# Kernel tuning notes

Hardware: AMD Instinct MI355X
Metric: run time of the kernel (lower is better)

The kernel has to match this reference:

```python
import jax, jax.numpy as jnp
import numpy as np

B, S, H, I, E, TOP_K = 2, 2048, 1024, 2048, 8, 2


def setup_inputs() -> dict:
    key = jax.random.key(0)
    k1, k2, k3, k4, k5 = jax.random.split(key, 5)
    scale_h = 1.0 / np.sqrt(H)
    scale_i = 1.0 / np.sqrt(I)
    return {
        "hidden_states": jax.random.normal(k1, (B, S, H), dtype=jnp.float32),
        "router_w": jax.random.normal(k2, (H, E), dtype=jnp.float32) * scale_h,
        "gate_w": jax.random.normal(k3, (E, H, I), dtype=jnp.float32) * scale_h,
        "up_w": jax.random.normal(k4, (E, H, I), dtype=jnp.float32) * scale_h,
        "out_w": jax.random.normal(k5, (E, I, H), dtype=jnp.float32) * scale_i,
    }


def reference(hidden_states, router_w, gate_w, up_w, out_w):
    b, s, h = hidden_states.shape
    x = hidden_states.reshape(-1, h)  # [T, H], T = B*S

    # Router: logits -> softmax -> top-k -> renormalize -> dense routing matrix
    router_logits = x @ router_w  # [T, E]
    router_probs = jax.nn.softmax(router_logits, axis=-1)
    top_p, top_i = jax.lax.top_k(router_probs, TOP_K)  # [T, K]
    top_p = top_p / jnp.sum(top_p, axis=-1, keepdims=True)
    one_hot = jax.nn.one_hot(top_i, E, dtype=top_p.dtype)  # [T, K, E]
    routing_full = jnp.sum(one_hot * top_p[..., None], axis=1)  # [T, E]
    routing_full = routing_full.T  # [E, T]

    # Dense all-expert FFN (SwiGLU), as in the original batched einsum form
    gate = jnp.einsum("th,ehm->etm", x, gate_w)  # [E, T, I]
    gate = jax.nn.silu(gate)
    intermediate = jnp.einsum("th,ehm->etm", x, up_w)  # [E, T, I]
    hidden = intermediate * gate
    expert_out = jnp.einsum("eti,eih->eth", hidden, out_w)  # [E, T, H]

    # Weighted combine over experts
    out = jnp.sum(expert_out * routing_full[:, :, None], axis=0)  # [T, H]
    out = out.reshape(b, s, h)
    return out, router_logits
```

## Files before the change

### kernel.cpp

```cpp
#include <hip/hip_runtime.h>
#include <hip/hip_bf16.h>
#include <stdint.h>

#define TT 4096
#define HH 1024
#define II 2048
#define EE 8
#define RB 16
#define NRB (TT / RB)
#define CSTRIDE 32

typedef short bf16x8 __attribute__((ext_vector_type(8)));
typedef float f32x4 __attribute__((ext_vector_type(4)));

__device__ __forceinline__ unsigned short f2bf(float f) {
  unsigned u = __float_as_uint(f);
  u += 0x7FFF + ((u >> 16) & 1);
  return (unsigned short)(u >> 16);
}

__device__ __forceinline__ void gl_lds16(const void* g, void* l) {
  auto gp = reinterpret_cast<const __attribute__((address_space(1))) unsigned int*>(
      reinterpret_cast<uintptr_t>(g));
  auto lp = reinterpret_cast<__attribute__((address_space(3))) unsigned int*>(
      reinterpret_cast<uintptr_t>(l));
  __builtin_amdgcn_global_load_lds(gp, lp, 16, 0, 0);
}

__device__ __forceinline__ void transpose_tile(const float* __restrict__ in,
                                               unsigned short* __restrict__ out,
                                               int M, int N, int mB, int nB,
                                               unsigned int* tl, int tid) {
  union F4 { float4 v; float f[4]; };
  int c4 = (tid & 15) * 4;
  int mp = tid >> 4;
#pragma unroll
  for (int it = 0; it < 2; ++it) {
    int m = (mp + it * 16) * 2;
    const float* p0 = in + (size_t)(mB + m) * N + nB + c4;
    F4 a, b;
    a.v = *(const float4*)p0;
    b.v = *(const float4*)(p0 + N);
    int mdw = m >> 1;
#pragma unroll
    for (int i = 0; i < 4; ++i) {
      int n = c4 + i;
      unsigned v = (unsigned)f2bf(a.f[i]) | ((unsigned)f2bf(b.f[i]) << 16);
      tl[n * 32 + ((mdw + n) & 31)] = v;
    }
  }
  __syncthreads();
  int n2 = tid >> 3;
  int md8 = (tid & 7) * 4;
#pragma unroll
  for (int it = 0; it < 2; ++it) {
    int n = n2 + it * 32;
    unsigned vv[4];
#pragma unroll
    for (int i = 0; i < 4; ++i)
      vv[i] = tl[n * 32 + ((md8 + i + n) & 31)];
    uint4 o4 = make_uint4(vv[0], vv[1], vv[2], vv[3]);
    *(uint4*)(out + (size_t)(nB + n) * M + mB + md8 * 2) = o4;
  }
}

__global__ void front_kernel(const float* __restrict__ x, const float* __restrict__ rw,
                             const float* __restrict__ gw, const float* __restrict__ uw,
                             float* __restrict__ logits_out, unsigned short* __restrict__ xb,
                             unsigned short* __restrict__ gwt, unsigned short* __restrict__ uwt,
                             int* __restrict__ gcnt, int2* __restrict__ ttop) {
  __shared__ unsigned int tl[2048];
  int b = blockIdx.x;
  int tid = threadIdx.x;

  if (b >= NRB) {
    int idx = b - NRB;
    int which = idx >> 12;
    int r = idx & 4095;
    int e = r >> 9;
    int tile = r & 511;
    int bx = tile & 31, by = tile >> 5;
    const float* in = (which ? uw : gw) + (size_t)e * HH * II;
    unsigned short* out = (which ? uwt : gwt) + (size_t)e * HH * II;
    transpose_tile(in, out, HH, II, by * 64, bx * 64, tl, tid);
    return;
  }

  __shared__ int bcnt[EE];
  int wave = tid >> 6, lane = tid & 63;
  if (tid < EE) bcnt[tid] = 0;
  __syncthreads();
  int t0 = b * RB;

  for (int sub = 0; sub < RB / 4; ++sub) {
    int li = sub * 4 + wave;
    int t = t0 + li;
    float acc[EE];
#pragma unroll
    for (int e = 0; e < EE; ++e) acc[e] = 0.f;
#pragma unroll
    for (int j = 0; j < 4; ++j) {
      int h = j * 256 + lane * 4;
      union F4 { float4 v; float f[4]; } xv;
      xv.v = *(const float4*)(x + (size_t)t * HH + h);
      union { unsigned short s[4]; uint2 v; } pk;
#pragma unroll
      for (int i = 0; i < 4; ++i) pk.s[i] = f2bf(xv.f[i]);
      *(uint2*)(xb + (size_t)t * HH + h) = pk.v;
#pragma unroll
      for (int i = 0; i < 4; ++i) {
        const float4* r4 = (const float4*)(rw + (h + i) * EE);
        float4 r0 = r4[0], r1 = r4[1];
        float xs = xv.f[i];
        acc[0] += xs * r0.x; acc[1] += xs * r0.y; acc[2] += xs * r0.z; acc[3] += xs * r0.w;
        acc[4] += xs * r1.x; acc[5] += xs * r1.y; acc[6] += xs * r1.z; acc[7] += xs * r1.w;
      }
    }
#pragma unroll
    for (int e = 0; e < EE; ++e)
#pragma unroll
      for (int off = 32; off; off >>= 1) acc[e] += __shfl_down(acc[e], off);
    if (lane == 0) {
      float4* lo = (float4*)(logits_out + (size_t)t * EE);
      lo[0] = make_float4(acc[0], acc[1], acc[2], acc[3]);
      lo[1] = make_float4(acc[4], acc[5], acc[6], acc[7]);
      int e0 = 0; float b0 = acc[0];
#pragma unroll
      for (int e = 1; e < EE; ++e) if (acc[e] > b0) { b0 = acc[e]; e0 = e; }
      int e1 = -1; float b1 = -3.4e38f;
#pragma unroll
      for (int e = 0; e < EE; ++e) if (e != e0 && acc[e] > b1) { b1 = acc[e]; e1 = e; }
      float w0 = 1.f / (1.f + __expf(b1 - b0));
      int lp0 = atomicAdd(&bcnt[e0], 1);
      int lp1 = atomicAdd(&bcnt[e1], 1);
      ttop[t] = make_int2(e0 | (e1 << 3) | (lp0 << 6) | (lp1 << 11), __float_as_int(w0));
    }
  }
  __syncthreads();
  if (tid < EE) gcnt[b * EE + tid] = bcnt[tid];
}

__global__ void scatter_kernel(const int* __restrict__ gcnt, const int2* __restrict__ ttop,
                               int* __restrict__ cnt, int* __restrict__ list,
                               int* __restrict__ tslot, float2* __restrict__ tw) {
  __shared__ int raw[NRB * EE];
  __shared__ int base[NRB][EE];
  int tid = threadIdx.x;
  for (int i = tid; i < NRB * EE; i += 256) raw[i] = gcnt[i];
  __syncthreads();
  if (tid < EE) {
    int s = 0;
    for (int b = 0; b < NRB; ++b) { base[b][tid] = s; s += raw[b * EE + tid]; }
    if (blockIdx.x == 0) cnt[tid * CSTRIDE] = s;
  }
  __syncthreads();
  int t = blockIdx.x * 256 + tid;
  int2 ti = ttop[t];
  int v = ti.x;
  float w0 = __int_as_float(ti.y);
  int e0 = v & 7, e1 = (v >> 3) & 7, lp0 = (v >> 6) & 31, lp1 = (v >> 11) & 31;
  int b = t >> 4;
  int p0 = base[b][e0] + lp0;
  int p1 = base[b][e1] + lp1;
  list[e0 * TT + p0] = t;
  list[e1 * TT + p1] = t;
  tslot[t * 2]     = (e0 << 16) | p0;
  tslot[t * 2 + 1] = (e1 << 16) | p1;
  tw[t] = make_float2(w0, 1.f - w0);
}

__launch_bounds__(256, 3)
__global__ void gemm1_kernel(const unsigned short* __restrict__ xb,
                             const unsigned short* __restrict__ gwt,
                             const unsigned short* __restrict__ uwt,
                             const float* __restrict__ ow, unsigned short* __restrict__ owt,
                             unsigned short* __restrict__ hidden,
                             const int* __restrict__ cnt, const int* __restrict__ list) {
  __shared__ __align__(16) unsigned short smem[16384];
  __shared__ int stok[128];
  int tid = threadIdx.x;
  int e = blockIdx.z;

  if (blockIdx.y >= 32) {
    int tile = (blockIdx.y - 32) * 32 + blockIdx.x;
    int bx = tile & 15, by = tile >> 4;
    transpose_tile(ow + (size_t)e * II * HH, owt + (size_t)e * II * HH,
                   II, HH, by * 64, bx * 64, (unsigned int*)smem, tid);
    return;
  }

  int cn = cnt[e * CSTRIDE];
  int hb0 = 0;
  for (int i = 0; i < EE; ++i) hb0 += (i < e) ? cnt[i * CSTRIDE] : 0;
  int mBase = blockIdx.y * 128;
  if (mBase >= cn) return;
  int nBase = blockIdx.x * 64;

  int wave = tid >> 6, lane = tid & 63;
  if (tid < 128) {
    int g = mBase + tid;
    stok[tid] = list[e * TT + (g < cn ? g : cn - 1)];
  }
  __syncthreads();

  const char* gaddr[8];
#pragma unroll
  for (int j = 0; j < 8; ++j) {
    int c = wave * 512 + j * 64 + lane;
    const char* g;
    if (c < 1024) {
      int r = c >> 3, sl = (c & 7) ^ (r & 7);
      g = (const char*)xb + (size_t)stok[r] * (HH * 2) + sl * 16;
    } else if (c < 1536) {
      int cc = c - 1024, r = cc >> 3, sl = (cc & 7) ^ (r & 7);
      g = (const char*)gwt + ((size_t)e * II + nBase + r) * (HH * 2) + sl * 16;
    } else {
      int cc = c - 1536, r = cc >> 3, sl = (cc & 7) ^ (r & 7);
      g = (const char*)uwt + ((size_t)e * II + nBase + r) * (HH * 2) + sl * 16;
    }
    gaddr[j] = g;
  }

  int q = lane >> 4, m16 = lane & 15;
  int wr = wave & 1, wc = wave >> 1;
  int faddrA[4][2], faddrBg[2][2], faddrBu[2][2];
#pragma unroll
  for (int mi = 0; mi < 4; ++mi) {
    int R = wr * 64 + mi * 16 + m16;
#pragma unroll
    for (int h = 0; h < 2; ++h)
      faddrA[mi][h] = (R * 8 + ((h * 4 + q) ^ (R & 7))) * 16;
  }
#pragma unroll
  for (int ni = 0; ni < 2; ++ni) {
    int n = wc * 32 + ni * 16 + m16;
#pragma unroll
    for (int h = 0; h < 2; ++h) {
      faddrBg[ni][h] = (1024 + n * 8 + ((h * 4 + q) ^ (n & 7))) * 16;
      faddrBu[ni][h] = (1536 + n * 8 + ((h * 4 + q) ^ (n & 7))) * 16;
    }
  }

  f32x4 zero4 = {0.f, 0.f, 0.f, 0.f};
  f32x4 accG[4][2], accU[4][2];
#pragma unroll
  for (int mi = 0; mi < 4; ++mi)
#pragma unroll
    for (int ni = 0; ni < 2; ++ni) { accG[mi][ni] = zero4; accU[mi][ni] = zero4; }

  const char* smemc = (const char*)smem;
  for (int kt = 0; kt < HH / 64; ++kt) {
    __syncthreads();
#pragma unroll
    for (int j = 0; j < 8; ++j) {
      gl_lds16(gaddr[j], (char*)smem + (size_t)(wave * 512 + j * 64) * 16);
      gaddr[j] += 128;
    }
    __syncthreads();
#pragma unroll
    for (int h = 0; h < 2; ++h) {
      bf16x8 aF[4], bG[2], bU[2];
#pragma unroll
      for (int mi = 0; mi < 4; ++mi) aF[mi] = *(const bf16x8*)(smemc + faddrA[mi][h]);
#pragma unroll
      for (int ni = 0; ni < 2; ++ni) {
        bG[ni] = *(const bf16x8*)(smemc + faddrBg[ni][h]);
        bU[ni] = *(const bf16x8*)(smemc + faddrBu[ni][h]);
      }
#pragma unroll
      for (int mi = 0; mi < 4; ++mi)
#pragma unroll
        for (int ni = 0; ni < 2; ++ni) {
          accG[mi][ni] = __builtin_amdgcn_mfma_f32_16x16x32_bf16(aF[mi], bG[ni], accG[mi][ni], 0, 0, 0);
          accU[mi][ni] = __builtin_amdgcn_mfma_f32_16x16x32_bf16(aF[mi], bU[ni], accU[mi][ni], 0, 0, 0);
        }
    }
  }

  int hb = hb0 + mBase;
  int rowsValid = cn - mBase; if (rowsValid > 128) rowsValid = 128;
#pragma unroll
  for (int mi = 0; mi < 4; ++mi)
#pragma unroll
    for (int ni = 0; ni < 2; ++ni)
#pragma unroll
      for (int r = 0; r < 4; ++r) {
        int row = wr * 64 + mi * 16 + q * 4 + r;
        if (row < rowsValid) {
          float g = accG[mi][ni][r], u = accU[mi][ni][r];
          float h = g / (1.f + __expf(-g)) * u;
          hidden[(size_t)(hb + row) * II + nBase + wc * 32 + ni * 16 + m16] = f2bf(h);
        }
      }
}

__launch_bounds__(256, 3)
__global__ void gemm2_kernel(const unsigned short* __restrict__ hidden,
                             const unsigned short* __restrict__ owt,
                             float* __restrict__ expert_out,
                             const int* __restrict__ cnt) {
  int e = blockIdx.z;
  int cn = cnt[e * CSTRIDE];
  int hb0 = 0;
  for (int i = 0; i < EE; ++i) hb0 += (i < e) ? cnt[i * CSTRIDE] : 0;
  int mBase = blockIdx.y * 128;
  if (mBase >= cn) return;
  int nBase = blockIdx.x * 64;

  __shared__ __align__(16) unsigned short smem[12288];

  int tid = threadIdx.x, wave = tid >> 6, lane = tid & 63;
  int hb = hb0 + mBase;
  const char* gaddr[6];
#pragma unroll
  for (int j = 0; j < 6; ++j) {
    int c = wave * 384 + j * 64 + lane;
    const char* g;
    if (c < 1024) {
      int r = c >> 3, sl = (c & 7) ^ (r & 7);
      g = (const char*)hidden + (size_t)(hb + r) * (II * 2) + sl * 16;
    } else {
      int cc = c - 1024, r = cc >> 3, sl = (cc & 7) ^ (r & 7);
      g = (const char*)owt + ((size_t)e * HH + nBase + r) * (II * 2) + sl * 16;
    }
    gaddr[j] = g;
  }

  int q = lane >> 4, m16 = lane & 15;
  int wr = wave & 1, wc = wave >> 1;
  int faddrA[4][2], faddrB[2][2];
#pragma unroll
  for (int mi = 0; mi < 4; ++mi) {
    int R = wr * 64 + mi * 16 + m16;
#pragma unroll
    for (int h = 0; h < 2; ++h)
      faddrA[mi][h] = (R * 8 + ((h * 4 + q) ^ (R & 7))) * 16;
  }
#pragma unroll
  for (int ni = 0; ni < 2; ++ni) {
    int n = wc * 32 + ni * 16 + m16;
#pragma unroll
    for (int h = 0; h < 2; ++h)
      faddrB[ni][h] = (1024 + n * 8 + ((h * 4 + q) ^ (n & 7))) * 16;
  }

  f32x4 zero4 = {0.f, 0.f, 0.f, 0.f};
  f32x4 acc[4][2];
#pragma unroll
  for (int mi = 0; mi < 4; ++mi)
#pragma unroll
    for (int ni = 0; ni < 2; ++ni) acc[mi][ni] = zero4;

  const char* smemc = (const char*)smem;
  for (int kt = 0; kt < II / 64; ++kt) {
    __syncthreads();
#pragma unroll
    for (int j = 0; j < 6; ++j) {
      gl_lds16(gaddr[j], (char*)smem + (size_t)(wave * 384 + j * 64) * 16);
      gaddr[j] += 128;
    }
    __syncthreads();
#pragma unroll
    for (int h = 0; h < 2; ++h) {
      bf16x8 aF[4], bF[2];
#pragma unroll
      for (int mi = 0; mi < 4; ++mi) aF[mi] = *(const bf16x8*)(smemc + faddrA[mi][h]);
#pragma unroll
      for (int ni = 0; ni < 2; ++ni) bF[ni] = *(const bf16x8*)(smemc + faddrB[ni][h]);
#pragma unroll
      for (int mi = 0; mi < 4; ++mi)
#pragma unroll
        for (int ni = 0; ni < 2; ++ni)
          acc[mi][ni] = __builtin_amdgcn_mfma_f32_16x16x32_bf16(aF[mi], bF[ni], acc[mi][ni], 0, 0, 0);
    }
  }

  int rowsValid = cn - mBase; if (rowsValid > 128) rowsValid = 128;
#pragma unroll
  for (int mi = 0; mi < 4; ++mi)
#pragma unroll
    for (int ni = 0; ni < 2; ++ni)
#pragma unroll
      for (int r = 0; r < 4; ++r) {
        int row = wr * 64 + mi * 16 + q * 4 + r;
        if (row < rowsValid)
          expert_out[(size_t)(hb + row) * HH + nBase + wc * 32 + ni * 16 + m16] = acc[mi][ni][r];
      }
}

__global__ void combine_kernel(const float* __restrict__ expert_out,
                               const int* __restrict__ cnt, const int* __restrict__ tslot,
                               const float2* __restrict__ tw, float* __restrict__ out) {
  int pre[EE];
  int s = 0;
#pragma unroll
  for (int e = 0; e < EE; ++e) { pre[e] = s; s += cnt[e * CSTRIDE]; }
  int t = blockIdx.x;
  int s0 = tslot[t * 2], s1 = tslot[t * 2 + 1];
  float2 w = tw[t];
  int r0 = pre[s0 >> 16] + (s0 & 0xFFFF);
  int r1 = pre[s1 >> 16] + (s1 & 0xFFFF);
  const float4* a = (const float4*)(expert_out + (size_t)r0 * HH);
  const float4* b = (const float4*)(expert_out + (size_t)r1 * HH);
  float4* o = (float4*)(out + (size_t)t * HH);
  int c = threadIdx.x;
  float4 av = a[c], bv = b[c];
  o[c] = make_float4(w.x * av.x + w.y * bv.x, w.x * av.y + w.y * bv.y,
                     w.x * av.z + w.y * bv.z, w.x * av.w + w.y * bv.w);
}

extern "C" void kernel_launch(void* const* d_in, const int* in_sizes, int n_in,
                              void* d_out, int out_size, void* d_ws, size_t ws_size,
                              hipStream_t stream) {
  (void)in_sizes; (void)n_in; (void)out_size; (void)ws_size;
  const float* x  = (const float*)d_in[0];
  const float* rw = (const float*)d_in[1];
  const float* gw = (const float*)d_in[2];
  const float* uw = (const float*)d_in[3];
  const float* ow = (const float*)d_in[4];
  float* out = (float*)d_out;
  float* logits = out + (size_t)TT * HH;

  char* ws = (char*)d_ws;
  size_t o = 0;
  auto alloc = [&](size_t bytes) {
    char* p = ws + o;
    o += (bytes + 255) & ~(size_t)255;
    return p;
  };
  unsigned short* xb  = (unsigned short*)alloc((size_t)TT * HH * 2);
  unsigned short* gwt = (unsigned short*)alloc((size_t)EE * II * HH * 2);
  unsigned short* uwt = (unsigned short*)alloc((size_t)EE * II * HH * 2);
  unsigned short* owt = (unsigned short*)alloc((size_t)EE * HH * II * 2);
  unsigned short* hidden = (unsigned short*)alloc((size_t)(2 * TT + 128) * II * 2);
  int*    cnt   = (int*)alloc(EE * CSTRIDE * 4);
  int*    list  = (int*)alloc((size_t)EE * TT * 4);
  int*    tslot = (int*)alloc((size_t)TT * 2 * 4);
  float2* tw    = (float2*)alloc((size_t)TT * 8);
  int*    gcnt  = (int*)alloc((size_t)NRB * EE * 4);
  int2*   ttop  = (int2*)alloc((size_t)TT * 8);
  float* expert_out = (float*)gwt;

  front_kernel<<<NRB + 8192, 256, 0, stream>>>(x, rw, gw, uw, logits, xb, gwt, uwt, gcnt, ttop);
  scatter_kernel<<<TT / 256, 256, 0, stream>>>(gcnt, ttop, cnt, list, tslot, tw);
  gemm1_kernel<<<dim3(32, 48, EE), 256, 0, stream>>>(xb, gwt, uwt, ow, owt, hidden, cnt, list);
  gemm2_kernel<<<dim3(HH / 64, TT / 128, EE), 256, 0, stream>>>(hidden, owt, expert_out, cnt);
  combine_kernel<<<TT, 256, 0, stream>>>(expert_out, cnt, tslot, tw, out);
}
```

Measured before the change: 403.6 us.

## Widen transpose tiles, move out_w transpose to front kernel, enlarge gemm2 N-tile

The weight-transpose helper now handles 64x128 tiles, issuing all eight global loads before converting, with a new LDS rotation pattern. The out_w transpose moves from extra gemm1 blocks into front_kernel, so all weight conversions run in one launch and gemm1 only launches GEMM blocks. gemm2's N tile doubles from 64 to 128, giving each wave a 4x4 MFMA accumulator grid for more reuse of A fragments. The cost is more registers and LDS per block and fewer blocks for gemm2, which may lower occupancy.

```diff
diff --git a/kernel.cpp b/kernel.cpp
--- a/kernel.cpp
+++ b/kernel.cpp
@@ -27,62 +27,74 @@
   __builtin_amdgcn_global_load_lds(gp, lp, 16, 0, 0);
 }
 
-__device__ __forceinline__ void transpose_tile(const float* __restrict__ in,
-                                               unsigned short* __restrict__ out,
-                                               int M, int N, int mB, int nB,
-                                               unsigned int* tl, int tid) {
+__device__ __forceinline__ void transpose_tile_wide(const float* __restrict__ in,
+                                                    unsigned short* __restrict__ out,
+                                                    int M, int N, int mB, int nB,
+                                                    unsigned int* tl, int tid) {
   union F4 { float4 v; float f[4]; };
-  int c4 = (tid & 15) * 4;
-  int mp = tid >> 4;
-#pragma unroll
-  for (int it = 0; it < 2; ++it) {
-    int m = (mp + it * 16) * 2;
-    const float* p0 = in + (size_t)(mB + m) * N + nB + c4;
-    F4 a, b;
-    a.v = *(const float4*)p0;
-    b.v = *(const float4*)(p0 + N);
-    int mdw = m >> 1;
+  int n4 = tid & 31;
+  int mph = tid >> 5;
+  F4 a[4], bq[4];
+  const float* base = in + (size_t)mB * N + nB + n4 * 4;
+#pragma unroll
+  for (int it = 0; it < 4; ++it) {
+    const float* p = base + (size_t)(2 * (mph + it * 8)) * N;
+    a[it].v = *(const float4*)p;
+    bq[it].v = *(const float4*)(p + N);
+  }
+#pragma unroll
+  for (int it = 0; it < 4; ++it) {
+    int mp = mph + it * 8;
 #pragma unroll
     for (int i = 0; i < 4; ++i) {
-      int n = c4 + i;
-      unsigned v = (unsigned)f2bf(a.f[i]) | ((unsigned)f2bf(b.f[i]) << 16);
-      tl[n * 32 + ((mdw + n) & 31)] = v;
-    }
-  }
-  __syncthreads();
-  int n2 = tid >> 3;
-  int md8 = (tid & 7) * 4;
-#pragma unroll
-  for (int it = 0; it < 2; ++it) {
-    int n = n2 + it * 32;
+      int n = n4 * 4 + i;
+      unsigned v = (unsigned)f2bf(a[it].f[i]) | ((unsigned)f2bf(bq[it].f[i]) << 16);
+      tl[n * 32 + ((mp + (n >> 2) + (n & 3)) & 31)] = v;
+    }
+  }
+  __syncthreads();
+  int md = tid & 7;
+  int nr = tid >> 3;
+#pragma unroll
+  for (int it = 0; it < 4; ++it) {
+    int n = nr + it * 32;
+    int rot = (n >> 2) + (n & 3);
     unsigned vv[4];
 #pragma unroll
-    for (int i = 0; i < 4; ++i)
-      vv[i] = tl[n * 32 + ((md8 + i + n) & 31)];
-    uint4 o4 = make_uint4(vv[0], vv[1], vv[2], vv[3]);
-    *(uint4*)(out + (size_t)(nB + n) * M + mB + md8 * 2) = o4;
-  }
-}
-
-__global__ void front_kernel(const float* __restrict__ x, const float* __restrict__ rw,
-                             const float* __restrict__ gw, const float* __restrict__ uw,
-                             float* __restrict__ logits_out, unsigned short* __restrict__ xb,
-                             unsigned short* __restrict__ gwt, unsigned short* __restrict__ uwt,
-                             int* __restrict__ gcnt, int2* __restrict__ ttop) {
-  __shared__ unsigned int tl[2048];
+    for (int k = 0; k < 4; ++k)
+      vv[k] = tl[n * 32 + ((md * 4 + k + rot) & 31)];
+    *(uint4*)(out + (size_t)(nB + n) * M + mB + md * 8) = make_uint4(vv[0], vv[1], vv[2], vv[3]);
+  }
+}
+
+__global__ __launch_bounds__(256, 4)
+void front_kernel(const float* __restrict__ x, const float* __restrict__ rw,
+                  const float* __restrict__ gw, const float* __restrict__ uw,
+                  const float* __restrict__ ow,
+                  float* __restrict__ logits_out, unsigned short* __restrict__ xb,
+                  unsigned short* __restrict__ gwt, unsigned short* __restrict__ uwt,
+                  unsigned short* __restrict__ owt,
+                  int* __restrict__ gcnt, int2* __restrict__ ttop) {
+  __shared__ unsigned int tl[4096];
   int b = blockIdx.x;
   int tid = threadIdx.x;
 
   if (b >= NRB) {
     int idx = b - NRB;
-    int which = idx >> 12;
-    int r = idx & 4095;
-    int e = r >> 9;
-    int tile = r & 511;
-    int bx = tile & 31, by = tile >> 5;
-    const float* in = (which ? uw : gw) + (size_t)e * HH * II;
-    unsigned short* out = (which ? uwt : gwt) + (size_t)e * HH * II;
-    transpose_tile(in, out, HH, II, by * 64, bx * 64, tl, tid);
+    int which = idx >> 11;
+    int r = idx & 2047;
+    int e = r >> 8;
+    int tile = r & 255;
+    if (which < 2) {
+      int bx = tile & 15, by = tile >> 4;
+      const float* in = (which ? uw : gw) + (size_t)e * HH * II;
+      unsigned short* o = (which ? uwt : gwt) + (size_t)e * HH * II;
+      transpose_tile_wide(in, o, HH, II, by * 64, bx * 128, tl, tid);
+    } else {
+      int bx = tile & 7, by = tile >> 3;
+      transpose_tile_wide(ow + (size_t)e * II * HH, owt + (size_t)e * II * HH,
+                          II, HH, by * 64, bx * 128, tl, tid);
+    }
     return;
   }
 
@@ -173,21 +185,12 @@
 __global__ void gemm1_kernel(const unsigned short* __restrict__ xb,
                              const unsigned short* __restrict__ gwt,
                              const unsigned short* __restrict__ uwt,
-                             const float* __restrict__ ow, unsigned short* __restrict__ owt,
                              unsigned short* __restrict__ hidden,
                              const int* __restrict__ cnt, const int* __restrict__ list) {
   __shared__ __align__(16) unsigned short smem[16384];
   __shared__ int stok[128];
   int tid = threadIdx.x;
   int e = blockIdx.z;
-
-  if (blockIdx.y >= 32) {
-    int tile = (blockIdx.y - 32) * 32 + blockIdx.x;
-    int bx = tile & 15, by = tile >> 4;
-    transpose_tile(ow + (size_t)e * II * HH, owt + (size_t)e * II * HH,
-                   II, HH, by * 64, bx * 64, (unsigned int*)smem, tid);
-    return;
-  }
 
   int cn = cnt[e * CSTRIDE];
   int hb0 = 0;
@@ -305,16 +308,16 @@
   for (int i = 0; i < EE; ++i) hb0 += (i < e) ? cnt[i * CSTRIDE] : 0;
   int mBase = blockIdx.y * 128;
   if (mBase >= cn) return;
-  int nBase = blockIdx.x * 64;
-
-  __shared__ __align__(16) unsigned short smem[12288];
+  int nBase = blockIdx.x * 128;
+
+  __shared__ __align__(16) unsigned short smem[16384];
 
   int tid = threadIdx.x, wave = tid >> 6, lane = tid & 63;
   int hb = hb0 + mBase;
-  const char* gaddr[6];
-#pragma unroll
-  for (int j = 0; j < 6; ++j) {
-    int c = wave * 384 + j * 64 + lane;
+  const char* gaddr[8];
+#pragma unroll
+  for (int j = 0; j < 8; ++j) {
+    int c = wave * 512 + j * 64 + lane;
     const char* g;
     if (c < 1024) {
       int r = c >> 3, sl = (c & 7) ^ (r & 7);
@@ -328,7 +331,7 @@
 
   int q = lane >> 4, m16 = lane & 15;
   int wr = wave & 1, wc = wave >> 1;
-  int faddrA[4][2], faddrB[2][2];
+  int faddrA[4][2], faddrB[4][2];
 #pragma unroll
   for (int mi = 0; mi < 4; ++mi) {
     int R = wr * 64 + mi * 16 + m16;
@@ -337,40 +340,40 @@
       faddrA[mi][h] = (R * 8 + ((h * 4 + q) ^ (R & 7))) * 16;
   }
 #pragma unroll
-  for (int ni = 0; ni < 2; ++ni) {
-    int n = wc * 32 + ni * 16 + m16;
+  for (int ni = 0; ni < 4; ++ni) {
+    int n = wc * 64 + ni * 16 + m16;
 #pragma unroll
     for (int h = 0; h < 2; ++h)
       faddrB[ni][h] = (1024 + n * 8 + ((h * 4 + q) ^ (n & 7))) * 16;
   }
 
   f32x4 zero4 = {0.f, 0.f, 0.f, 0.f};
-  f32x4 acc[4][2];
+  f32x4 acc[4][4];
 #pragma unroll
   for (int mi = 0; mi < 4; ++mi)
 #pragma unroll
-    for (int ni = 0; ni < 2; ++ni) acc[mi][ni] = zero4;
+    for (int ni = 0; ni < 4; ++ni) acc[mi][ni] = zero4;
 
   const char* smemc = (const char*)smem;
   for (int kt = 0; kt < II / 64; ++kt) {
     __syncthreads();
 #pragma unroll
-    for (int j = 0; j < 6; ++j) {
-      gl_lds16(gaddr[j], (char*)smem + (size_t)(wave * 384 + j * 64) * 16);
+    for (int j = 0; j < 8; ++j) {
+      gl_lds16(gaddr[j], (char*)smem + (size_t)(wave * 512 + j * 64) * 16);
       gaddr[j] += 128;
     }
     __syncthreads();
 #pragma unroll
     for (int h = 0; h < 2; ++h) {
-      bf16x8 aF[4], bF[2];
+      bf16x8 aF[4], bF[4];
 #pragma unroll
       for (int mi = 0; mi < 4; ++mi) aF[mi] = *(const bf16x8*)(smemc + faddrA[mi][h]);
 #pragma unroll
-      for (int ni = 0; ni < 2; ++ni) bF[ni] = *(const bf16x8*)(smemc + faddrB[ni][h]);
+      for (int ni = 0; ni < 4; ++ni) bF[ni] = *(const bf16x8*)(smemc + faddrB[ni][h]);
 #pragma unroll
       for (int mi = 0; mi < 4; ++mi)
 #pragma unroll
-        for (int ni = 0; ni < 2; ++ni)
+        for (int ni = 0; ni < 4; ++ni)
           acc[mi][ni] = __builtin_amdgcn_mfma_f32_16x16x32_bf16(aF[mi], bF[ni], acc[mi][ni], 0, 0, 0);
     }
   }
@@ -379,12 +382,12 @@
 #pragma unroll
   for (int mi = 0; mi < 4; ++mi)
 #pragma unroll
-    for (int ni = 0; ni < 2; ++ni)
+    for (int ni = 0; ni < 4; ++ni)
 #pragma unroll
       for (int r = 0; r < 4; ++r) {
         int row = wr * 64 + mi * 16 + q * 4 + r;
         if (row < rowsValid)
-          expert_out[(size_t)(hb + row) * HH + nBase + wc * 32 + ni * 16 + m16] = acc[mi][ni][r];
+          expert_out[(size_t)(hb + row) * HH + nBase + wc * 64 + ni * 16 + m16] = acc[mi][ni][r];
       }
 }
 
@@ -441,9 +444,10 @@
   int2*   ttop  = (int2*)alloc((size_t)TT * 8);
   float* expert_out = (float*)gwt;
 
-  front_kernel<<<NRB + 8192, 256, 0, stream>>>(x, rw, gw, uw, logits, xb, gwt, uwt, gcnt, ttop);
+  front_kernel<<<NRB + 3 * 2048, 256, 0, stream>>>(x, rw, gw, uw, ow, logits, xb, gwt, uwt, owt,
+                                                   gcnt, ttop);
   scatter_kernel<<<TT / 256, 256, 0, stream>>>(gcnt, ttop, cnt, list, tslot, tw);
-  gemm1_kernel<<<dim3(32, 48, EE), 256, 0, stream>>>(xb, gwt, uwt, ow, owt, hidden, cnt, list);
-  gemm2_kernel<<<dim3(HH / 64, TT / 128, EE), 256, 0, stream>>>(hidden, owt, expert_out, cnt);
+  gemm1_kernel<<<dim3(32, 32, EE), 256, 0, stream>>>(xb, gwt, uwt, hidden, cnt, list);
+  gemm2_kernel<<<dim3(HH / 128, TT / 128, EE), 256, 0, stream>>>(hidden, owt, expert_out, cnt);
   combine_kernel<<<TT, 256, 0, stream>>>(expert_out, cnt, tslot, tw, out);
 }
```

New measurement: 398.9 us. No clear change (-1.2%).
